# Performance work log

Hardware: AMD Instinct MI355X
Metric: run time of the kernel (lower is better)

## Reference

```python
import jax, jax.numpy as jnp
import numpy as np

N_NODES = 50000
N_EDGES = 800000
N_POS = 200000
N_NEG = 200000
D_IN = 128
D_OUT = 128
NEG_SLOPE = 0.2  # DGL GATConv default leaky_relu slope


def setup_inputs() -> dict:
    key = jax.random.key(0)
    ks = jax.random.split(key, 12)
    inp = {
        "x": jax.random.normal(ks[0], (N_NODES, D_IN), dtype=jnp.float32),
        "W": jax.random.normal(ks[1], (D_IN, D_OUT), dtype=jnp.float32) / np.sqrt(D_IN),
        "attn_l": jax.random.normal(ks[2], (D_OUT,), dtype=jnp.float32) / np.sqrt(D_OUT),
        "attn_r": jax.random.normal(ks[3], (D_OUT,), dtype=jnp.float32) / np.sqrt(D_OUT),
        "bias": jnp.zeros((D_OUT,), dtype=jnp.float32),
        "src": jax.random.randint(ks[4], (N_EDGES,), 0, N_NODES, dtype=jnp.int32),
        "dst": jax.random.randint(ks[5], (N_EDGES,), 0, N_NODES, dtype=jnp.int32),
        "pos_src": jax.random.randint(ks[6], (N_POS,), 0, N_NODES, dtype=jnp.int32),
        "pos_dst": jax.random.randint(ks[7], (N_POS,), 0, N_NODES, dtype=jnp.int32),
        "neg_src": jax.random.randint(ks[8], (N_NEG,), 0, N_NODES, dtype=jnp.int32),
        "neg_dst": jax.random.randint(ks[9], (N_NEG,), 0, N_NODES, dtype=jnp.int32),
    }
    return inp


def _gat_conv(x, W, attn_l, attn_r, bias, src, dst):
    # DGL GATConv, num_heads=1, feat_drop=0, activation=relu
    feat = x @ W                               # [N, D_OUT]
    el = feat @ attn_l                         # [N]
    er = feat @ attn_r                         # [N]
    e = jax.nn.leaky_relu(el[src] + er[dst], NEG_SLOPE)  # [E]
    # edge softmax grouped by destination node
    m = jax.ops.segment_max(e, dst, num_segments=N_NODES)   # [N]
    ee = jnp.exp(e - m[dst])
    s = jax.ops.segment_sum(ee, dst, num_segments=N_NODES)  # [N]
    a = ee / s[dst]                            # [E]
    # weighted message aggregation
    h = jax.ops.segment_sum(a[:, None] * feat[src], dst, num_segments=N_NODES)
    return jax.nn.relu(h + bias)               # [N, D_OUT]


def reference(x, W, attn_l, attn_r, bias, src, dst, pos_src, pos_dst, neg_src, neg_dst):
    h = _gat_conv(x, W, attn_l, attn_r, bias, src, dst)
    # ScorePredictor: u_dot_v on each scoring graph -> [E, 1]
    pos_score = jnp.sum(h[pos_src] * h[pos_dst], axis=-1, keepdims=True)
    neg_score = jnp.sum(h[neg_src] * h[neg_dst], axis=-1, keepdims=True)
    return (pos_score, neg_score)
```

## Files before the change

### kernel.cpp

```cpp
#include <hip/hip_runtime.h>
#include <hip/hip_bf16.h>
#include <cstdint>
#include <cstddef>

#define N_NODES 50000
#define N_EDGES 800000
#define N_POS   200000
#define N_NEG   200000
#define DIM     128
#define NEG_SLOPE 0.2f

#define BUCK_SHIFT 5
#define BUCK_NODES 32
#define NBUCK 1563
#define SLABCAP 768
#define BIN_CHUNK 4096
#define NB_BIN 196

typedef _Float16 half8 __attribute__((ext_vector_type(8)));

__global__ __launch_bounds__(256) void gemm_feat(
    const float* __restrict__ x, const float* __restrict__ W,
    const float* __restrict__ attn_l, const float* __restrict__ attn_r,
    half8* __restrict__ feat16, float* __restrict__ el, float* __restrict__ er,
    int n)
{
  __shared__ float xs[64][33];
  __shared__ float ws[32][128];
  const int tid = threadIdx.x;
  const int row0 = blockIdx.x * 64;
  const int rg = tid & 15;
  const int cg = tid >> 4;

  float acc[4][8];
#pragma unroll
  for (int i = 0; i < 4; ++i)
#pragma unroll
    for (int j = 0; j < 8; ++j) acc[i][j] = 0.f;

  for (int kc = 0; kc < DIM; kc += 32) {
    {
      const int r = tid >> 2;
      const int c = (tid & 3) * 8;
      const int grow = row0 + r;
      float4 v0 = make_float4(0.f, 0.f, 0.f, 0.f);
      float4 v1 = make_float4(0.f, 0.f, 0.f, 0.f);
      if (grow < n) {
        const float* srcp = &x[(size_t)grow * DIM + kc + c];
        v0 = *(const float4*)(srcp);
        v1 = *(const float4*)(srcp + 4);
      }
      xs[r][c + 0] = v0.x; xs[r][c + 1] = v0.y; xs[r][c + 2] = v0.z; xs[r][c + 3] = v0.w;
      xs[r][c + 4] = v1.x; xs[r][c + 5] = v1.y; xs[r][c + 6] = v1.z; xs[r][c + 7] = v1.w;
    }
    {
      const int r = tid >> 3;
      const int c = (tid & 7) * 16;
      const float* srcp = &W[(size_t)(kc + r) * DIM + c];
      *(float4*)&ws[r][c + 0]  = *(const float4*)(srcp + 0);
      *(float4*)&ws[r][c + 4]  = *(const float4*)(srcp + 4);
      *(float4*)&ws[r][c + 8]  = *(const float4*)(srcp + 8);
      *(float4*)&ws[r][c + 12] = *(const float4*)(srcp + 12);
    }
    __syncthreads();
#pragma unroll 8
    for (int k = 0; k < 32; ++k) {
      const float a0 = xs[rg * 4 + 0][k];
      const float a1 = xs[rg * 4 + 1][k];
      const float a2 = xs[rg * 4 + 2][k];
      const float a3 = xs[rg * 4 + 3][k];
      const float4 w0 = *(const float4*)&ws[k][cg * 8];
      const float4 w1 = *(const float4*)&ws[k][cg * 8 + 4];
      const float wv[8] = {w0.x, w0.y, w0.z, w0.w, w1.x, w1.y, w1.z, w1.w};
#pragma unroll
      for (int j = 0; j < 8; ++j) {
        acc[0][j] = fmaf(a0, wv[j], acc[0][j]);
        acc[1][j] = fmaf(a1, wv[j], acc[1][j]);
        acc[2][j] = fmaf(a2, wv[j], acc[2][j]);
        acc[3][j] = fmaf(a3, wv[j], acc[3][j]);
      }
    }
    __syncthreads();
  }

#pragma unroll
  for (int i = 0; i < 4; ++i) {
    const int grow = row0 + rg * 4 + i;
    if (grow < n) {
      half8 o;
#pragma unroll
      for (int j = 0; j < 8; ++j) o[j] = (_Float16)acc[i][j];
      feat16[(size_t)grow * 16 + cg] = o;
    }
  }

  const float4 al0 = *(const float4*)&attn_l[cg * 8];
  const float4 al1 = *(const float4*)&attn_l[cg * 8 + 4];
  const float4 ar0 = *(const float4*)&attn_r[cg * 8];
  const float4 ar1 = *(const float4*)&attn_r[cg * 8 + 4];
  const float alv[8] = {al0.x, al0.y, al0.z, al0.w, al1.x, al1.y, al1.z, al1.w};
  const float arv[8] = {ar0.x, ar0.y, ar0.z, ar0.w, ar1.x, ar1.y, ar1.z, ar1.w};
  float* redl = &ws[0][0];
  float* redr = redl + 64 * 17;
#pragma unroll
  for (int i = 0; i < 4; ++i) {
    float pl = 0.f, pr = 0.f;
#pragma unroll
    for (int j = 0; j < 8; ++j) {
      pl = fmaf(acc[i][j], alv[j], pl);
      pr = fmaf(acc[i][j], arv[j], pr);
    }
    redl[(rg * 4 + i) * 17 + cg] = pl;
    redr[(rg * 4 + i) * 17 + cg] = pr;
  }
  __syncthreads();
  if (tid < 64) {
    const int grow = row0 + tid;
    if (grow < n) {
      float sl = 0.f, sr = 0.f;
#pragma unroll
      for (int c = 0; c < 16; ++c) {
        sl += redl[tid * 17 + c];
        sr += redr[tid * 17 + c];
      }
      el[grow] = sl;
      er[grow] = sr;
    }
  }
}

__global__ __launch_bounds__(256) void bin_kernel(
    const int* __restrict__ src, const int* __restrict__ dst,
    unsigned int* __restrict__ slab, int* __restrict__ slab_cursor)
{
  __shared__ int hist[NBUCK];
  __shared__ int base_s[NBUCK];
  __shared__ int cur[NBUCK];
  const int tid = threadIdx.x;
  const int e0 = blockIdx.x * BIN_CHUNK;
  for (int i = tid; i < NBUCK; i += 256) { hist[i] = 0; cur[i] = 0; }
  __syncthreads();
  for (int i = tid; i < BIN_CHUNK; i += 256) {
    const int e = e0 + i;
    if (e < N_EDGES) atomicAdd(&hist[dst[e] >> BUCK_SHIFT], 1);
  }
  __syncthreads();
  for (int i = tid; i < NBUCK; i += 256) {
    const int h = hist[i];
    base_s[i] = h ? atomicAdd(&slab_cursor[i], h) : 0;
  }
  __syncthreads();
  for (int i = tid; i < BIN_CHUNK; i += 256) {
    const int e = e0 + i;
    if (e >= N_EDGES) continue;
    const int d = dst[e];
    const int bk = d >> BUCK_SHIFT;
    const int p = atomicAdd(&cur[bk], 1);
    int idx = base_s[bk] + p;
    if (idx >= SLABCAP) idx = SLABCAP - 1;
    slab[(size_t)bk * SLABCAP + idx] =
        ((unsigned int)src[e] << BUCK_SHIFT) | (unsigned int)(d & (BUCK_NODES - 1));
  }
}

__global__ __launch_bounds__(256) void aggregate_kernel(
    const half8* __restrict__ feat16, const float* __restrict__ el,
    const float* __restrict__ er,
    const unsigned int* __restrict__ slab, const int* __restrict__ slab_cursor,
    const float* __restrict__ bias, half8* __restrict__ h16)
{
  __shared__ unsigned int csr[SLABCAP];
  __shared__ int cnt_l[BUCK_NODES];
  __shared__ int start_l[BUCK_NODES];
  __shared__ int cur_l[BUCK_NODES];
  const int b = blockIdx.x;
  const int tid = threadIdx.x;
  const int cnt = min(slab_cursor[b], SLABCAP);
  const unsigned int* sb = slab + (size_t)b * SLABCAP;
  const int node0 = b << BUCK_SHIFT;

  if (tid < BUCK_NODES) cnt_l[tid] = 0;
  __syncthreads();
  for (int i = tid; i < cnt; i += 256)
    atomicAdd(&cnt_l[sb[i] & (BUCK_NODES - 1)], 1);
  __syncthreads();
  if (tid < 64) {
    const int v = (tid < BUCK_NODES) ? cnt_l[tid] : 0;
    int inc = v;
#pragma unroll
    for (int d = 1; d < 32; d <<= 1) {
      const int t = __shfl_up(inc, d, 64);
      if (tid >= d) inc += t;
    }
    if (tid < BUCK_NODES) { start_l[tid] = inc - v; cur_l[tid] = 0; }
  }
  __syncthreads();
  for (int i = tid; i < cnt; i += 256) {
    const unsigned int r = sb[i];
    const int p = atomicAdd(&cur_l[r & (BUCK_NODES - 1)], 1);
    csr[start_l[r & (BUCK_NODES - 1)] + p] = r;
  }
  __syncthreads();

  const int lane = tid & 63;
  const int ql = lane & 15;
  const int qb = lane & 48;
  const int qid = (tid >> 6) * 4 + (lane >> 4);
  const float4 b0 = *(const float4*)&bias[ql * 8];
  const float4 b1 = *(const float4*)&bias[ql * 8 + 4];
  const float bb[8] = {b0.x, b0.y, b0.z, b0.w, b1.x, b1.y, b1.z, b1.w};

  for (int nl = qid; nl < BUCK_NODES; nl += 16) {
    const int node = node0 + nl;
    if (node >= N_NODES) break;
    const int beg = start_l[nl];
    const int c = cnt_l[nl];
    const float ern = er[node];

    float sp = 0.f;
    float acc[8];
#pragma unroll
    for (int k = 0; k < 8; ++k) acc[k] = 0.f;

    for (int t0 = 0; t0 < c; t0 += 16) {
      const int t = t0 + ql;
      const unsigned int r = csr[beg + ((t < c) ? t : (c - 1))];
      const int sid = (int)(r >> BUCK_SHIFT);
      float w = 0.f;
      if (t < c) {
        const float v = el[sid] + ern;
        const float e = (v > 0.f) ? v : NEG_SLOPE * v;
        w = __expf(e);
      }
      sp += w;
      const int nb = min(16, c - t0);
      int j = 0;
      for (; j + 4 <= nb; j += 4) {
        float wv[4]; int sv[4]; half8 fv[4];
#pragma unroll
        for (int u = 0; u < 4; ++u) {
          wv[u] = __shfl(w, qb + j + u, 64);
          sv[u] = __shfl(sid, qb + j + u, 64);
        }
#pragma unroll
        for (int u = 0; u < 4; ++u) fv[u] = feat16[(size_t)sv[u] * 16 + ql];
#pragma unroll
        for (int u = 0; u < 4; ++u)
#pragma unroll
          for (int k = 0; k < 8; ++k)
            acc[k] = fmaf(wv[u], (float)fv[u][k], acc[k]);
      }
      for (; j < nb; ++j) {
        const float wj = __shfl(w, qb + j, 64);
        const int sj = __shfl(sid, qb + j, 64);
        const half8 f = feat16[(size_t)sj * 16 + ql];
#pragma unroll
        for (int k = 0; k < 8; ++k) acc[k] = fmaf(wj, (float)f[k], acc[k]);
      }
    }

#pragma unroll
    for (int o = 1; o < 16; o <<= 1) sp += __shfl_xor(sp, o, 64);

    const float inv = (c > 0) ? 1.f / sp : 0.f;
    half8 o;
#pragma unroll
    for (int k = 0; k < 8; ++k)
      o[k] = (_Float16)fmaxf(acc[k] * inv + bb[k], 0.f);
    h16[(size_t)node * 16 + ql] = o;
  }
}

__global__ __launch_bounds__(256) void score_kernel(
    const half8* __restrict__ h16,
    const int* __restrict__ pos_src, const int* __restrict__ pos_dst,
    const int* __restrict__ neg_src, const int* __restrict__ neg_dst,
    float* __restrict__ out, int ntot)
{
  const int wid = (int)((blockIdx.x * blockDim.x + threadIdx.x) >> 6);
  const int lane = threadIdx.x & 63;
  const int q = lane >> 4;
  const int ql = lane & 15;
  const int base = (wid * 4 + q) * 4;

  int av[4], bv[4];
#pragma unroll
  for (int u = 0; u < 4; ++u) {
    const int p = base + u;
    int a = 0, b = 0;
    if (p < N_POS)      { a = pos_src[p]; b = pos_dst[p]; }
    else if (p < ntot)  { a = neg_src[p - N_POS]; b = neg_dst[p - N_POS]; }
    av[u] = a; bv[u] = b;
  }
  half8 ha[4], hb[4];
#pragma unroll
  for (int u = 0; u < 4; ++u) {
    ha[u] = h16[(size_t)av[u] * 16 + ql];
    hb[u] = h16[(size_t)bv[u] * 16 + ql];
  }
  float sum[4];
#pragma unroll
  for (int u = 0; u < 4; ++u) {
    float s = 0.f;
#pragma unroll
    for (int k = 0; k < 8; ++k) s = fmaf((float)ha[u][k], (float)hb[u][k], s);
#pragma unroll
    for (int o = 8; o > 0; o >>= 1) s += __shfl_xor(s, o, 64);
    sum[u] = s;
  }
  if (ql == 0) {
#pragma unroll
    for (int u = 0; u < 4; ++u) {
      const int p = base + u;
      if (p < ntot) out[p] = sum[u];
    }
  }
}

extern "C" void kernel_launch(void* const* d_in, const int* in_sizes, int n_in,
                              void* d_out, int out_size, void* d_ws, size_t ws_size,
                              hipStream_t stream) {
  const float* x      = (const float*)d_in[0];
  const float* W      = (const float*)d_in[1];
  const float* attn_l = (const float*)d_in[2];
  const float* attn_r = (const float*)d_in[3];
  const float* bias   = (const float*)d_in[4];
  const int* src      = (const int*)d_in[5];
  const int* dst      = (const int*)d_in[6];
  const int* pos_src  = (const int*)d_in[7];
  const int* pos_dst  = (const int*)d_in[8];
  const int* neg_src  = (const int*)d_in[9];
  const int* neg_dst  = (const int*)d_in[10];
  float* out = (float*)d_out;

  char* ws = (char*)d_ws;
  const size_t F16B = (size_t)N_NODES * DIM * sizeof(_Float16);
  half8* feat16          = (half8*)(ws);
  half8* h16             = (half8*)(ws + F16B);
  float* el              = (float*)(ws + 2 * F16B);
  float* er              = (float*)(ws + 2 * F16B + 200000);
  int*   slab_cursor     = (int*)  (ws + 2 * F16B + 400000);
  unsigned int* slab     = (unsigned int*)(ws + 2 * F16B + 406656);

  hipMemsetAsync(slab_cursor, 0, NBUCK * sizeof(int), stream);

  gemm_feat<<<(N_NODES + 63) / 64, 256, 0, stream>>>(
      x, W, attn_l, attn_r, feat16, el, er, N_NODES);
  bin_kernel<<<NB_BIN, 256, 0, stream>>>(src, dst, slab, slab_cursor);
  aggregate_kernel<<<NBUCK, 256, 0, stream>>>(
      feat16, el, er, slab, slab_cursor, bias, h16);
  score_kernel<<<((N_POS + N_NEG + 15) / 16 + 3) / 4, 256, 0, stream>>>(
      h16, pos_src, pos_dst, neg_src, neg_dst, out, N_POS + N_NEG);
}
```

Measured before the change: 202.8 us.

## Use MFMA f16 matrix cores for feature GEMM and double bin chunk size

Replaces the scalar FP32 FMA tiled GEMM with MFMA 16x16x32 f16 instructions. x and W are converted to half and staged in XOR-swizzled shared memory, and el/er are computed with wave shuffle reductions. Output is transposed through shared memory so feat16 can be written with coalesced stores. The binning kernel's chunk size is also doubled, halving its block count. Rounding x and W to fp16 before the multiply adds precision error, and the larger shared memory footprint (48KB) may lower occupancy.

New measurement: 201.1 us. No clear change (-0.8%).

```diff
diff --git a/kernel.cpp b/kernel.cpp
--- a/kernel.cpp
+++ b/kernel.cpp
@@ -14,10 +14,11 @@
 #define BUCK_NODES 32
 #define NBUCK 1563
 #define SLABCAP 768
-#define BIN_CHUNK 4096
-#define NB_BIN 196
+#define BIN_CHUNK 8192
+#define NB_BIN 98
 
 typedef _Float16 half8 __attribute__((ext_vector_type(8)));
+typedef float    floatx4 __attribute__((ext_vector_type(4)));
 
 __global__ __launch_bounds__(256) void gemm_feat(
     const float* __restrict__ x, const float* __restrict__ W,
@@ -25,106 +26,124 @@
     half8* __restrict__ feat16, float* __restrict__ el, float* __restrict__ er,
     int n)
 {
-  __shared__ float xs[64][33];
-  __shared__ float ws[32][128];
+  __shared__ _Float16 xt[64 * 128];
+  __shared__ _Float16 wt[128 * 128];
   const int tid = threadIdx.x;
   const int row0 = blockIdx.x * 64;
-  const int rg = tid & 15;
-  const int cg = tid >> 4;
-
-  float acc[4][8];
-#pragma unroll
-  for (int i = 0; i < 4; ++i)
-#pragma unroll
-    for (int j = 0; j < 8; ++j) acc[i][j] = 0.f;
-
-  for (int kc = 0; kc < DIM; kc += 32) {
-    {
-      const int r = tid >> 2;
-      const int c = (tid & 3) * 8;
-      const int grow = row0 + r;
+  const int lane = tid & 63;
+  const int wv = tid >> 6;
+  const int ql = lane & 15;
+  const int quad = lane >> 4;
+
+  {
+    const int k = tid >> 1;
+    const int n0 = (tid & 1) * 64;
+#pragma unroll 4
+    for (int j = 0; j < 64; j += 4) {
+      const float4 v = *(const float4*)&W[(size_t)k * DIM + n0 + j];
+      const float vv[4] = {v.x, v.y, v.z, v.w};
+#pragma unroll
+      for (int u = 0; u < 4; ++u) {
+        const int nn = n0 + j + u;
+        wt[nn * 128 + ((((k >> 3) ^ (nn & 15)) << 3) | (k & 7))] = (_Float16)vv[u];
+      }
+    }
+  }
+  {
+    const int r = tid >> 2;
+    const int grow = row0 + r;
+    const int c0 = (tid & 3) * 32;
+#pragma unroll
+    for (int cc = 0; cc < 32; cc += 8) {
+      const int c = c0 + cc;
       float4 v0 = make_float4(0.f, 0.f, 0.f, 0.f);
       float4 v1 = make_float4(0.f, 0.f, 0.f, 0.f);
       if (grow < n) {
-        const float* srcp = &x[(size_t)grow * DIM + kc + c];
-        v0 = *(const float4*)(srcp);
-        v1 = *(const float4*)(srcp + 4);
-      }
-      xs[r][c + 0] = v0.x; xs[r][c + 1] = v0.y; xs[r][c + 2] = v0.z; xs[r][c + 3] = v0.w;
-      xs[r][c + 4] = v1.x; xs[r][c + 5] = v1.y; xs[r][c + 6] = v1.z; xs[r][c + 7] = v1.w;
-    }
-    {
-      const int r = tid >> 3;
-      const int c = (tid & 7) * 16;
-      const float* srcp = &W[(size_t)(kc + r) * DIM + c];
-      *(float4*)&ws[r][c + 0]  = *(const float4*)(srcp + 0);
-      *(float4*)&ws[r][c + 4]  = *(const float4*)(srcp + 4);
-      *(float4*)&ws[r][c + 8]  = *(const float4*)(srcp + 8);
-      *(float4*)&ws[r][c + 12] = *(const float4*)(srcp + 12);
-    }
-    __syncthreads();
-#pragma unroll 8
-    for (int k = 0; k < 32; ++k) {
-      const float a0 = xs[rg * 4 + 0][k];
-      const float a1 = xs[rg * 4 + 1][k];
-      const float a2 = xs[rg * 4 + 2][k];
-      const float a3 = xs[rg * 4 + 3][k];
-      const float4 w0 = *(const float4*)&ws[k][cg * 8];
-      const float4 w1 = *(const float4*)&ws[k][cg * 8 + 4];
-      const float wv[8] = {w0.x, w0.y, w0.z, w0.w, w1.x, w1.y, w1.z, w1.w};
-#pragma unroll
-      for (int j = 0; j < 8; ++j) {
-        acc[0][j] = fmaf(a0, wv[j], acc[0][j]);
-        acc[1][j] = fmaf(a1, wv[j], acc[1][j]);
-        acc[2][j] = fmaf(a2, wv[j], acc[2][j]);
-        acc[3][j] = fmaf(a3, wv[j], acc[3][j]);
-      }
-    }
-    __syncthreads();
-  }
-
-#pragma unroll
-  for (int i = 0; i < 4; ++i) {
-    const int grow = row0 + rg * 4 + i;
+        const float* sp = &x[(size_t)grow * DIM + c];
+        v0 = *(const float4*)(sp);
+        v1 = *(const float4*)(sp + 4);
+      }
+      half8 h;
+      h[0] = (_Float16)v0.x; h[1] = (_Float16)v0.y;
+      h[2] = (_Float16)v0.z; h[3] = (_Float16)v0.w;
+      h[4] = (_Float16)v1.x; h[5] = (_Float16)v1.y;
+      h[6] = (_Float16)v1.z; h[7] = (_Float16)v1.w;
+      const int chunk = c >> 3;
+      *(half8*)&xt[r * 128 + ((chunk ^ (r & 15)) << 3)] = h;
+    }
+  }
+  __syncthreads();
+
+  floatx4 acc[8];
+#pragma unroll
+  for (int t = 0; t < 8; ++t) acc[t] = (floatx4){0.f, 0.f, 0.f, 0.f};
+
+  const int arow = wv * 16 + ql;
+  half8 af[4];
+#pragma unroll
+  for (int s = 0; s < 4; ++s) {
+    const int chunk = s * 4 + quad;
+    af[s] = *(half8*)&xt[arow * 128 + ((chunk ^ ql) << 3)];
+  }
+#pragma unroll
+  for (int t = 0; t < 8; ++t) {
+    const int brow = t * 16 + ql;
+#pragma unroll
+    for (int s = 0; s < 4; ++s) {
+      const int chunk = s * 4 + quad;
+      const half8 bf = *(half8*)&wt[brow * 128 + ((chunk ^ ql) << 3)];
+      acc[t] = __builtin_amdgcn_mfma_f32_16x16x32_f16(af[s], bf, acc[t], 0, 0, 0);
+    }
+  }
+
+  {
+    float al8[8], ar8[8];
+#pragma unroll
+    for (int t = 0; t < 8; ++t) {
+      al8[t] = attn_l[t * 16 + ql];
+      ar8[t] = attn_r[t * 16 + ql];
+    }
+    float pl[4] = {0.f, 0.f, 0.f, 0.f};
+    float pr[4] = {0.f, 0.f, 0.f, 0.f};
+#pragma unroll
+    for (int t = 0; t < 8; ++t)
+#pragma unroll
+      for (int r = 0; r < 4; ++r) {
+        pl[r] = fmaf(acc[t][r], al8[t], pl[r]);
+        pr[r] = fmaf(acc[t][r], ar8[t], pr[r]);
+      }
+#pragma unroll
+    for (int o = 1; o < 16; o <<= 1)
+#pragma unroll
+      for (int r = 0; r < 4; ++r) {
+        pl[r] += __shfl_xor(pl[r], o, 64);
+        pr[r] += __shfl_xor(pr[r], o, 64);
+      }
+    if (ql == 0) {
+#pragma unroll
+      for (int r = 0; r < 4; ++r) {
+        const int grow = row0 + wv * 16 + quad * 4 + r;
+        if (grow < n) { el[grow] = pl[r]; er[grow] = pr[r]; }
+      }
+    }
+  }
+
+#pragma unroll
+  for (int t = 0; t < 8; ++t)
+#pragma unroll
+    for (int r = 0; r < 4; ++r)
+      xt[(wv * 16 + quad * 4 + r) * 128 + t * 16 + ql] = (_Float16)acc[t][r];
+  __syncthreads();
+  {
+    const int r = tid >> 2;
+    const int grow = row0 + r;
     if (grow < n) {
-      half8 o;
-#pragma unroll
-      for (int j = 0; j < 8; ++j) o[j] = (_Float16)acc[i][j];
-      feat16[(size_t)grow * 16 + cg] = o;
-    }
-  }
-
-  const float4 al0 = *(const float4*)&attn_l[cg * 8];
-  const float4 al1 = *(const float4*)&attn_l[cg * 8 + 4];
-  const float4 ar0 = *(const float4*)&attn_r[cg * 8];
-  const float4 ar1 = *(const float4*)&attn_r[cg * 8 + 4];
-  const float alv[8] = {al0.x, al0.y, al0.z, al0.w, al1.x, al1.y, al1.z, al1.w};
-  const float arv[8] = {ar0.x, ar0.y, ar0.z, ar0.w, ar1.x, ar1.y, ar1.z, ar1.w};
-  float* redl = &ws[0][0];
-  float* redr = redl + 64 * 17;
-#pragma unroll
-  for (int i = 0; i < 4; ++i) {
-    float pl = 0.f, pr = 0.f;
-#pragma unroll
-    for (int j = 0; j < 8; ++j) {
-      pl = fmaf(acc[i][j], alv[j], pl);
-      pr = fmaf(acc[i][j], arv[j], pr);
-    }
-    redl[(rg * 4 + i) * 17 + cg] = pl;
-    redr[(rg * 4 + i) * 17 + cg] = pr;
-  }
-  __syncthreads();
-  if (tid < 64) {
-    const int grow = row0 + tid;
-    if (grow < n) {
-      float sl = 0.f, sr = 0.f;
-#pragma unroll
-      for (int c = 0; c < 16; ++c) {
-        sl += redl[tid * 17 + c];
-        sr += redr[tid * 17 + c];
-      }
-      el[grow] = sl;
-      er[grow] = sr;
+      const int c0 = (tid & 3) * 32;
+#pragma unroll
+      for (int cc = 0; cc < 32; cc += 8) {
+        const half8 h = *(half8*)&xt[r * 128 + c0 + cc];
+        feat16[(size_t)grow * 16 + ((c0 + cc) >> 3)] = h;
+      }
     }
   }
 }
```
